# Performance work log

Hardware: AMD Instinct MI355X
Metric: run time of the kernel (lower is better)

The kernel has to match this reference:

```python
import jax, jax.numpy as jnp
import numpy as np

N, C, H = 256, 128, 4
D = C // H


def setup_inputs() -> dict:
    key = jax.random.key(0)
    ks = jax.random.split(key, 7)
    pair_rep = jax.random.normal(ks[0], (N, N, C), dtype=jnp.float32)
    distance_matrix = jax.random.normal(ks[1], (N, N), dtype=jnp.float32)
    Wqkv = jax.random.normal(ks[2], (C, 3 * C), dtype=jnp.float32) * (1.0 / np.sqrt(C))
    bqkv = jax.random.normal(ks[3], (3 * C,), dtype=jnp.float32) * 0.02
    Wout = jax.random.normal(ks[4], (C, C), dtype=jnp.float32) * (1.0 / np.sqrt(C))
    bout = jax.random.normal(ks[5], (C,), dtype=jnp.float32) * 0.02
    dscale = jnp.ones((1,), dtype=jnp.float32)
    mask = jax.random.randint(ks[6], (N, N), 0, 2).astype(jnp.bool_)
    return {"pair_rep": pair_rep, "distance_matrix": distance_matrix, "Wqkv": Wqkv,
            "bqkv": bqkv, "Wout": Wout, "bout": bout, "dscale": dscale, "mask": mask}


def reference(pair_rep, distance_matrix, Wqkv, bqkv, Wout, bout, dscale, mask):
    n = pair_rep.shape[0]
    qkv = pair_rep @ Wqkv + bqkv                      # [n,n,3c]
    q, k, v = jnp.split(qkv, 3, axis=-1)
    q = q.reshape(n, n, H, D)
    k = k.reshape(n, n, H, D)
    v = v.reshape(n, n, H, D)
    # scores[h,i,j,k] = q[i,j,h,:] . k[i,k,h,:] / sqrt(D)
    scores = jnp.einsum('ijhd,ikhd->hijk', q, k) / np.sqrt(D)
    bias = (dscale[0] * distance_matrix)[None, None, :, :]   # [1,1,n,n]
    scores = scores + bias
    scores = jnp.where(mask[None, None, :, :], -jnp.inf, scores)
    attn = jax.nn.softmax(scores, axis=-1)            # [H,n,n,n]
    out = jnp.einsum('hijk,ikhd->ijhd', attn, v).reshape(n, n, C)
    return out @ Wout + bout
```

## Files before the change

kernel.cpp:

```cpp
#include <hip/hip_runtime.h>
#include <hip/hip_bf16.h>
#include <math.h>

#define NN 256
#define CC 128
#define HH 4
#define DD 32

typedef uint4 u128;
typedef __bf16 bf16x8 __attribute__((ext_vector_type(8)));
typedef float f32x4 __attribute__((ext_vector_type(4)));

#define LOG2E 1.4426950408889634f
#define QSC (0.17677669529663687f * LOG2E)

__global__ __launch_bounds__(256) void prep_kernel(
    const float* __restrict__ dm, const int* __restrict__ mask,
    const float* __restrict__ dscale,
    const float* __restrict__ Wqkv, const float* __restrict__ Wout,
    float* __restrict__ biasM,
    __hip_bfloat16* __restrict__ Wt_qkv, __hip_bfloat16* __restrict__ Wt_out)
{
    const int b = blockIdx.x, t = threadIdx.x;
    if (b < 256) {
        int idx = b * 256 + t;
        biasM[idx] = mask[idx] ? -INFINITY : dscale[0] * dm[idx] * LOG2E;
    } else if (b < 448) {
        int idx = (b - 256) * 256 + t;
        int n = idx >> 7, k = idx & 127;
        Wt_qkv[idx] = __float2bfloat16(Wqkv[(size_t)k * 384 + n]);
    } else {
        int idx = (b - 448) * 256 + t;
        int n = idx >> 7, k = idx & 127;
        Wt_out[idx] = __float2bfloat16(Wout[(size_t)k * CC + n]);
    }
}

__global__ __launch_bounds__(512, 4) void qkv_mfma_kernel(
    const float* __restrict__ A,
    const __hip_bfloat16* __restrict__ Bt,
    const float* __restrict__ bias,
    __hip_bfloat16* __restrict__ out)
{
    __shared__ __align__(16) __hip_bfloat16 As[128][136];
    __shared__ __align__(16) __hip_bfloat16 Bs[96][136];
    const int t = threadIdx.x;
    const int m0 = blockIdx.x * 128;
    const int n0 = blockIdx.y * 96;

    #pragma unroll
    for (int it = 0; it < 8; ++it) {
        int idx = it * 512 + t;
        int r = idx >> 5, c4 = (idx & 31) * 4;
        float4 v = *(const float4*)(A + (size_t)(m0 + r) * CC + c4);
        __hip_bfloat162 a01 = __float22bfloat162_rn(float2{v.x, v.y});
        __hip_bfloat162 a23 = __float22bfloat162_rn(float2{v.z, v.w});
        uint2 pk;
        pk.x = *(unsigned int*)&a01;
        pk.y = *(unsigned int*)&a23;
        *(uint2*)&As[r][c4] = pk;
    }
    #pragma unroll
    for (int it = 0; it < 3; ++it) {
        int idx = it * 512 + t;
        int n = idx >> 4, c8 = (idx & 15) * 8;
        *(u128*)&Bs[n][c8] = *(const u128*)(Bt + (size_t)(n0 + n) * CC + c8);
    }
    __syncthreads();

    const int w = t >> 6, lane = t & 63;
    const int n16 = lane & 15, quad = lane >> 4;
    const int mw = (w & 3) * 32, nw = (w >> 2) * 48;

    bf16x8 pf[2][4];
    #pragma unroll
    for (int mt = 0; mt < 2; ++mt)
        #pragma unroll
        for (int ks = 0; ks < 4; ++ks)
            pf[mt][ks] = *(const bf16x8*)&As[mw + mt * 16 + n16][ks * 32 + quad * 8];

    f32x4 acc[2][3];
    #pragma unroll
    for (int mt = 0; mt < 2; ++mt)
        #pragma unroll
        for (int nt = 0; nt < 3; ++nt) acc[mt][nt] = (f32x4){0.f, 0.f, 0.f, 0.f};

    #pragma unroll
    for (int nt = 0; nt < 3; ++nt) {
        bf16x8 wf[4];
        #pragma unroll
        for (int ks = 0; ks < 4; ++ks)
            wf[ks] = *(const bf16x8*)&Bs[nw + nt * 16 + n16][ks * 32 + quad * 8];
        #pragma unroll
        for (int ks = 0; ks < 4; ++ks)
            #pragma unroll
            for (int mt = 0; mt < 2; ++mt)
                acc[mt][nt] = __builtin_amdgcn_mfma_f32_16x16x32_bf16(wf[ks], pf[mt][ks], acc[mt][nt], 0, 0, 0);
    }

    #pragma unroll
    for (int nt = 0; nt < 3; ++nt) {
        int nbase = n0 + nw + nt * 16 + quad * 4;
        float4 b4 = *(const float4*)(bias + nbase);
        float sc = (nbase < CC) ? QSC : 1.0f;
        #pragma unroll
        for (int mt = 0; mt < 2; ++mt) {
            int m = m0 + mw + mt * 16 + n16;
            __hip_bfloat162 h01 = __float22bfloat162_rn(float2{(acc[mt][nt][0] + b4.x) * sc, (acc[mt][nt][1] + b4.y) * sc});
            __hip_bfloat162 h23 = __float22bfloat162_rn(float2{(acc[mt][nt][2] + b4.z) * sc, (acc[mt][nt][3] + b4.w) * sc});
            uint2 pk;
            pk.x = *(unsigned int*)&h01;
            pk.y = *(unsigned int*)&h23;
            *(uint2*)&out[(size_t)m * 384 + nbase] = pk;
        }
    }
}

__global__ __launch_bounds__(512, 4) void attn_mfma_kernel(
    const __hip_bfloat16* __restrict__ qkv,
    const float* __restrict__ biasM,
    __hip_bfloat16* __restrict__ attn_out)
{
    __shared__ __align__(16) __hip_bfloat16 Ks[NN][40];
    __shared__ __align__(16) __hip_bfloat16 VTs[DD][264];
    __shared__ __align__(16) __hip_bfloat16 Ps[8][16][136];

    const int bi = blockIdx.x;
    const int i = bi >> 2, h = bi & 3;
    const int t = threadIdx.x;

    if (t < NN) {
        const __hip_bfloat16* base = qkv + (size_t)(i * NN + t) * 384 + h * DD;
        const u128* ksrc = (const u128*)(base + CC);
        const u128* vsrc = (const u128*)(base + 2 * CC);
        u128* kdst = (u128*)&Ks[t][0];
        u128 vr[4];
        #pragma unroll
        for (int u = 0; u < 4; ++u) { kdst[u] = ksrc[u]; vr[u] = vsrc[u]; }
        const __hip_bfloat16* vh = (const __hip_bfloat16*)vr;
        #pragma unroll
        for (int d = 0; d < DD; ++d) VTs[d][t] = vh[d];
    }
    __syncthreads();

    const int w = t >> 6, lane = t & 63;
    const int n16 = lane & 15, quad = lane >> 4;

    for (int jt = 0; jt < 2; ++jt) {
        const int j0 = w * 32 + jt * 16;
        const int j = j0 + n16;

        bf16x8 qa = *(const bf16x8*)(qkv + (size_t)(i * NN + j) * 384 + h * DD + quad * 8);
        const float4* brow = (const float4*)(biasM + (size_t)j * NN);

        f32x4 s[16];
        #pragma unroll
        for (int kt = 0; kt < 16; ++kt) {
            bf16x8 kb = *(const bf16x8*)&Ks[kt * 16 + n16][quad * 8];
            float4 b4 = brow[kt * 4 + quad];
            s[kt] = __builtin_amdgcn_mfma_f32_16x16x32_bf16(
                kb, qa, (f32x4){b4.x, b4.y, b4.z, b4.w}, 0, 0, 0);
        }

        f32x4 sm = {0.f, 0.f, 0.f, 0.f};
        f32x4 o[2] = {(f32x4){0.f, 0.f, 0.f, 0.f}, (f32x4){0.f, 0.f, 0.f, 0.f}};
        #pragma unroll
        for (int pass = 0; pass < 2; ++pass) {
            #pragma unroll
            for (int kt8 = 0; kt8 < 8; ++kt8) {
                int kt = pass * 8 + kt8;
                float p0 = exp2f(s[kt][0]);
                float p1 = exp2f(s[kt][1]);
                float p2 = exp2f(s[kt][2]);
                float p3 = exp2f(s[kt][3]);
                sm[0] += p0; sm[1] += p1; sm[2] += p2; sm[3] += p3;
                __hip_bfloat162 h01 = __float22bfloat162_rn(float2{p0, p1});
                __hip_bfloat162 h23 = __float22bfloat162_rn(float2{p2, p3});
                uint2 pk;
                pk.x = *(unsigned int*)&h01;
                pk.y = *(unsigned int*)&h23;
                *(uint2*)&Ps[w][n16][kt8 * 16 + quad * 4] = pk;
            }
            #pragma unroll
            for (int c = 0; c < 4; ++c) {
                bf16x8 pa = *(const bf16x8*)&Ps[w][n16][c * 32 + quad * 8];
                #pragma unroll
                for (int dt = 0; dt < 2; ++dt) {
                    bf16x8 vb = *(const bf16x8*)&VTs[dt * 16 + n16][pass * 128 + c * 32 + quad * 8];
                    o[dt] = __builtin_amdgcn_mfma_f32_16x16x32_bf16(vb, pa, o[dt], 0, 0, 0);
                }
            }
        }
        float sum = (sm[0] + sm[1]) + (sm[2] + sm[3]);
        sum += __shfl_xor(sum, 16);
        sum += __shfl_xor(sum, 32);
        float inv = 1.0f / sum;

        __hip_bfloat16* obase = attn_out + (size_t)(i * NN + j) * CC + h * DD + quad * 4;
        #pragma unroll
        for (int dt = 0; dt < 2; ++dt) {
            __hip_bfloat162 h01 = __float22bfloat162_rn(float2{o[dt][0] * inv, o[dt][1] * inv});
            __hip_bfloat162 h23 = __float22bfloat162_rn(float2{o[dt][2] * inv, o[dt][3] * inv});
            uint2 pk;
            pk.x = *(unsigned int*)&h01;
            pk.y = *(unsigned int*)&h23;
            *(uint2*)(obase + dt * 16) = pk;
        }
    }
}

__global__ __launch_bounds__(512, 4) void out_mfma_kernel(
    const __hip_bfloat16* __restrict__ A,
    const __hip_bfloat16* __restrict__ Bt,
    const float* __restrict__ bias,
    float* __restrict__ out)
{
    __shared__ __align__(16) __hip_bfloat16 As[128][136];
    __shared__ __align__(16) __hip_bfloat16 Bs[128][136];
    const int t = threadIdx.x;
    const int m0 = blockIdx.x * 128;

    #pragma unroll
    for (int it = 0; it < 4; ++it) {
        int idx = it * 512 + t;
        int r = idx >> 4, c8 = (idx & 15) * 8;
        *(u128*)&As[r][c8] = *(const u128*)(A + (size_t)(m0 + r) * CC + c8);
    }
    #pragma unroll
    for (int it = 0; it < 4; ++it) {
        int idx = it * 512 + t;
        int n = idx >> 4, c8 = (idx & 15) * 8;
        *(u128*)&Bs[n][c8] = *(const u128*)(Bt + (size_t)n * CC + c8);
    }
    __syncthreads();

    const int w = t >> 6, lane = t & 63;
    const int n16 = lane & 15, quad = lane >> 4;
    const int mw = (w & 3) * 32, nw = (w >> 2) * 64;

    bf16x8 pf[2][4];
    #pragma unroll
    for (int mt = 0; mt < 2; ++mt)
        #pragma unroll
        for (int ks = 0; ks < 4; ++ks)
            pf[mt][ks] = *(const bf16x8*)&As[mw + mt * 16 + n16][ks * 32 + quad * 8];

    f32x4 acc[2][4];
    #pragma unroll
    for (int mt = 0; mt < 2; ++mt)
        #pragma unroll
        for (int nt = 0; nt < 4; ++nt) acc[mt][nt] = (f32x4){0.f, 0.f, 0.f, 0.f};

    #pragma unroll
    for (int nt = 0; nt < 4; ++nt) {
        bf16x8 wf[4];
        #pragma unroll
        for (int ks = 0; ks < 4; ++ks)
            wf[ks] = *(const bf16x8*)&Bs[nw + nt * 16 + n16][ks * 32 + quad * 8];
        #pragma unroll
        for (int ks = 0; ks < 4; ++ks)
            #pragma unroll
            for (int mt = 0; mt < 2; ++mt)
                acc[mt][nt] = __builtin_amdgcn_mfma_f32_16x16x32_bf16(wf[ks], pf[mt][ks], acc[mt][nt], 0, 0, 0);
    }

    #pragma unroll
    for (int nt = 0; nt < 4; ++nt) {
        int nbase = nw + nt * 16 + quad * 4;
        float4 b4 = *(const float4*)(bias + nbase);
        #pragma unroll
        for (int mt = 0; mt < 2; ++mt) {
            int m = m0 + mw + mt * 16 + n16;
            float4 ov;
            ov.x = acc[mt][nt][0] + b4.x;
            ov.y = acc[mt][nt][1] + b4.y;
            ov.z = acc[mt][nt][2] + b4.z;
            ov.w = acc[mt][nt][3] + b4.w;
            *(float4*)&out[(size_t)m * CC + nbase] = ov;
        }
    }
}

extern "C" void kernel_launch(void* const* d_in, const int* in_sizes, int n_in,
                              void* d_out, int out_size, void* d_ws, size_t ws_size,
                              hipStream_t stream) {
    const float* pair_rep = (const float*)d_in[0];
    const float* dm       = (const float*)d_in[1];
    const float* Wqkv     = (const float*)d_in[2];
    const float* bqkv     = (const float*)d_in[3];
    const float* Wout     = (const float*)d_in[4];
    const float* bout     = (const float*)d_in[5];
    const float* dscale   = (const float*)d_in[6];
    const int*   mask     = (const int*)d_in[7];
    float* out = (float*)d_out;

    char* p = (char*)d_ws;
    float* biasM = (float*)p;                 p += (size_t)NN * NN * 4;
    __hip_bfloat16* Wt_qkv = (__hip_bfloat16*)p;  p += (size_t)384 * CC * 2;
    __hip_bfloat16* Wt_out = (__hip_bfloat16*)p;  p += (size_t)CC * CC * 2;
    __hip_bfloat16* qkv  = (__hip_bfloat16*)p;    p += (size_t)65536 * 384 * 2;
    __hip_bfloat16* attn = (__hip_bfloat16*)p;

    prep_kernel<<<dim3(512), dim3(256), 0, stream>>>(dm, mask, dscale, Wqkv, Wout, biasM, Wt_qkv, Wt_out);
    qkv_mfma_kernel<<<dim3(512, 4), dim3(512), 0, stream>>>(pair_rep, Wt_qkv, bqkv, qkv);
    attn_mfma_kernel<<<dim3(1024), dim3(512), 0, stream>>>(qkv, biasM, attn);
    out_mfma_kernel<<<dim3(512), dim3(512), 0, stream>>>(attn, Wt_out, bout, out);
}
```

Baseline: 175.3 us.

## Pre-convert pair_rep to bf16, spread K/V staging, raise MFMA priority

The prep kernel now also converts pair_rep from fp32 to bf16 into the attn workspace buffer. Before, each of the four qkv GEMM column blocks reloaded and converted the fp32 rows on its own; now it loads bf16 tiles with 128-bit loads. The attention kernel stages K/V with all 512 threads instead of 256, separates the bias loads from the QK MFMAs, wraps the MFMA loops in s_setprio, and uses the raw exp2 intrinsic. The cost is an extra full-size bf16 write and read of the input, and the raw exp2 may handle denormals or edge cases differently.

```diff
diff --git a/kernel.cpp b/kernel.cpp
--- a/kernel.cpp
+++ b/kernel.cpp
@@ -18,8 +18,10 @@
     const float* __restrict__ dm, const int* __restrict__ mask,
     const float* __restrict__ dscale,
     const float* __restrict__ Wqkv, const float* __restrict__ Wout,
+    const float* __restrict__ pair,
     float* __restrict__ biasM,
-    __hip_bfloat16* __restrict__ Wt_qkv, __hip_bfloat16* __restrict__ Wt_out)
+    __hip_bfloat16* __restrict__ Wt_qkv, __hip_bfloat16* __restrict__ Wt_out,
+    __hip_bfloat16* __restrict__ Abf)
 {
     const int b = blockIdx.x, t = threadIdx.x;
     if (b < 256) {
@@ -29,15 +31,29 @@
         int idx = (b - 256) * 256 + t;
         int n = idx >> 7, k = idx & 127;
         Wt_qkv[idx] = __float2bfloat16(Wqkv[(size_t)k * 384 + n]);
-    } else {
+    } else if (b < 512) {
         int idx = (b - 448) * 256 + t;
         int n = idx >> 7, k = idx & 127;
         Wt_out[idx] = __float2bfloat16(Wout[(size_t)k * CC + n]);
+    } else {
+        size_t e = (size_t)(b - 512) * 2048 + (size_t)t * 8;
+        float4 v0 = *(const float4*)(pair + e);
+        float4 v1 = *(const float4*)(pair + e + 4);
+        __hip_bfloat162 a01 = __float22bfloat162_rn(float2{v0.x, v0.y});
+        __hip_bfloat162 a23 = __float22bfloat162_rn(float2{v0.z, v0.w});
+        __hip_bfloat162 a45 = __float22bfloat162_rn(float2{v1.x, v1.y});
+        __hip_bfloat162 a67 = __float22bfloat162_rn(float2{v1.z, v1.w});
+        u128 pk;
+        pk.x = *(unsigned int*)&a01;
+        pk.y = *(unsigned int*)&a23;
+        pk.z = *(unsigned int*)&a45;
+        pk.w = *(unsigned int*)&a67;
+        *(u128*)&Abf[e] = pk;
     }
 }
 
 __global__ __launch_bounds__(512, 4) void qkv_mfma_kernel(
-    const float* __restrict__ A,
+    const __hip_bfloat16* __restrict__ A,
     const __hip_bfloat16* __restrict__ Bt,
     const float* __restrict__ bias,
     __hip_bfloat16* __restrict__ out)
@@ -49,16 +65,10 @@
     const int n0 = blockIdx.y * 96;
 
     #pragma unroll
-    for (int it = 0; it < 8; ++it) {
+    for (int it = 0; it < 4; ++it) {
         int idx = it * 512 + t;
-        int r = idx >> 5, c4 = (idx & 31) * 4;
-        float4 v = *(const float4*)(A + (size_t)(m0 + r) * CC + c4);
-        __hip_bfloat162 a01 = __float22bfloat162_rn(float2{v.x, v.y});
-        __hip_bfloat162 a23 = __float22bfloat162_rn(float2{v.z, v.w});
-        uint2 pk;
-        pk.x = *(unsigned int*)&a01;
-        pk.y = *(unsigned int*)&a23;
-        *(uint2*)&As[r][c4] = pk;
+        int r = idx >> 4, c8 = (idx & 15) * 8;
+        *(u128*)&As[r][c8] = *(const u128*)(A + (size_t)(m0 + r) * CC + c8);
     }
     #pragma unroll
     for (int it = 0; it < 3; ++it) {
@@ -129,17 +139,20 @@
     const int i = bi >> 2, h = bi & 3;
     const int t = threadIdx.x;
 
-    if (t < NN) {
-        const __hip_bfloat16* base = qkv + (size_t)(i * NN + t) * 384 + h * DD;
-        const u128* ksrc = (const u128*)(base + CC);
-        const u128* vsrc = (const u128*)(base + 2 * CC);
-        u128* kdst = (u128*)&Ks[t][0];
-        u128 vr[4];
-        #pragma unroll
-        for (int u = 0; u < 4; ++u) { kdst[u] = ksrc[u]; vr[u] = vsrc[u]; }
+    {
+        const int r = t >> 1, half = t & 1;
+        const __hip_bfloat16* base = qkv + (size_t)(i * NN + r) * 384 + h * DD;
+        const u128* ksrc = (const u128*)(base + CC) + half * 2;
+        u128* kdst = (u128*)&Ks[r][0] + half * 2;
+        kdst[0] = ksrc[0];
+        kdst[1] = ksrc[1];
+        const u128* vsrc = (const u128*)(base + 2 * CC) + half * 2;
+        u128 vr[2];
+        vr[0] = vsrc[0];
+        vr[1] = vsrc[1];
         const __hip_bfloat16* vh = (const __hip_bfloat16*)vr;
         #pragma unroll
-        for (int d = 0; d < DD; ++d) VTs[d][t] = vh[d];
+        for (int dd = 0; dd < 16; ++dd) VTs[half * 16 + dd][r] = vh[dd];
     }
     __syncthreads();
 
@@ -156,11 +169,16 @@
         f32x4 s[16];
         #pragma unroll
         for (int kt = 0; kt < 16; ++kt) {
+            float4 b4 = brow[kt * 4 + quad];
+            s[kt] = (f32x4){b4.x, b4.y, b4.z, b4.w};
+        }
+        __builtin_amdgcn_s_setprio(1);
+        #pragma unroll
+        for (int kt = 0; kt < 16; ++kt) {
             bf16x8 kb = *(const bf16x8*)&Ks[kt * 16 + n16][quad * 8];
-            float4 b4 = brow[kt * 4 + quad];
-            s[kt] = __builtin_amdgcn_mfma_f32_16x16x32_bf16(
-                kb, qa, (f32x4){b4.x, b4.y, b4.z, b4.w}, 0, 0, 0);
-        }
+            s[kt] = __builtin_amdgcn_mfma_f32_16x16x32_bf16(kb, qa, s[kt], 0, 0, 0);
+        }
+        __builtin_amdgcn_s_setprio(0);
 
         f32x4 sm = {0.f, 0.f, 0.f, 0.f};
         f32x4 o[2] = {(f32x4){0.f, 0.f, 0.f, 0.f}, (f32x4){0.f, 0.f, 0.f, 0.f}};
@@ -169,10 +187,10 @@
             #pragma unroll
             for (int kt8 = 0; kt8 < 8; ++kt8) {
                 int kt = pass * 8 + kt8;
-                float p0 = exp2f(s[kt][0]);
-                float p1 = exp2f(s[kt][1]);
-                float p2 = exp2f(s[kt][2]);
-                float p3 = exp2f(s[kt][3]);
+                float p0 = __builtin_amdgcn_exp2f(s[kt][0]);
+                float p1 = __builtin_amdgcn_exp2f(s[kt][1]);
+                float p2 = __builtin_amdgcn_exp2f(s[kt][2]);
+                float p3 = __builtin_amdgcn_exp2f(s[kt][3]);
                 sm[0] += p0; sm[1] += p1; sm[2] += p2; sm[3] += p3;
                 __hip_bfloat162 h01 = __float22bfloat162_rn(float2{p0, p1});
                 __hip_bfloat162 h23 = __float22bfloat162_rn(float2{p2, p3});
@@ -181,6 +199,7 @@
                 pk.y = *(unsigned int*)&h23;
                 *(uint2*)&Ps[w][n16][kt8 * 16 + quad * 4] = pk;
             }
+            __builtin_amdgcn_s_setprio(1);
             #pragma unroll
             for (int c = 0; c < 4; ++c) {
                 bf16x8 pa = *(const bf16x8*)&Ps[w][n16][c * 32 + quad * 8];
@@ -190,6 +209,7 @@
                     o[dt] = __builtin_amdgcn_mfma_f32_16x16x32_bf16(vb, pa, o[dt], 0, 0, 0);
                 }
             }
+            __builtin_amdgcn_s_setprio(0);
         }
         float sum = (sm[0] + sm[1]) + (sm[2] + sm[3]);
         sum += __shfl_xor(sum, 16);
@@ -300,9 +320,10 @@
     __hip_bfloat16* Wt_out = (__hip_bfloat16*)p;  p += (size_t)CC * CC * 2;
     __hip_bfloat16* qkv  = (__hip_bfloat16*)p;    p += (size_t)65536 * 384 * 2;
     __hip_bfloat16* attn = (__hip_bfloat16*)p;
-
-    prep_kernel<<<dim3(512), dim3(256), 0, stream>>>(dm, mask, dscale, Wqkv, Wout, biasM, Wt_qkv, Wt_out);
-    qkv_mfma_kernel<<<dim3(512, 4), dim3(512), 0, stream>>>(pair_rep, Wt_qkv, bqkv, qkv);
+    __hip_bfloat16* Abf  = attn;
+
+    prep_kernel<<<dim3(4608), dim3(256), 0, stream>>>(dm, mask, dscale, Wqkv, Wout, pair_rep, biasM, Wt_qkv, Wt_out, Abf);
+    qkv_mfma_kernel<<<dim3(512, 4), dim3(512), 0, stream>>>(Abf, Wt_qkv, bqkv, qkv);
     attn_mfma_kernel<<<dim3(1024), dim3(512), 0, stream>>>(qkv, biasM, attn);
     out_mfma_kernel<<<dim3(512), dim3(512), 0, stream>>>(attn, Wt_out, bout, out);
 }
```

New measurement: 169.7 us. -3.2%, faster.
